# Kernel tuning notes

Hardware: AMD Instinct MI355X
Metric: run time of the kernel (lower is better)

Reference implementation:

```python
import jax, jax.numpy as jnp
import numpy as np

B, N, NODE_DIM = 64, 64, 192
H = 256          # node_hidden_dim
PDIM = 64        # property_embedding_dim
NUM_EDGE_TYPE = 5
T = 4            # message-passing rounds
E = 16384        # total edges (flattened batched graph)
E_SEL = 65536    # selected candidate pairs


def setup_inputs() -> dict:
    key = jax.random.key(0)
    ks = jax.random.split(key, 24)
    def g(k, shape, scale=0.05):
        return jax.random.normal(k, shape, dtype=jnp.float32) * scale
    inp = {
        "x": jax.random.normal(ks[0], (B, N, NODE_DIM), dtype=jnp.float32),
        "edge_index": jax.random.randint(ks[1], (2, E), 0, B * N, dtype=jnp.int32),
        "edge_attr": jax.random.uniform(ks[2], (E, NUM_EDGE_TYPE), dtype=jnp.float32),
        "props": jax.random.normal(ks[3], (B, 1), dtype=jnp.float32),
        "sel_b": jax.random.randint(ks[4], (E_SEL,), 0, B, dtype=jnp.int32),
        "sel_i": jax.random.randint(ks[5], (E_SEL,), 0, N, dtype=jnp.int32),
        "sel_j": jax.random.randint(ks[6], (E_SEL,), 0, N, dtype=jnp.int32),
        "golden_edge": jax.random.randint(ks[7], (E_SEL,), 0, NUM_EDGE_TYPE, dtype=jnp.int32),
        # parameters
        "W_prop": g(ks[8], (1, PDIM)), "b_prop": jnp.zeros((PDIM,), jnp.float32),
        "W_in": g(ks[9], (NODE_DIM, H)), "b_in": jnp.zeros((H,), jnp.float32),
        "W_msg": g(ks[10], (H + NUM_EDGE_TYPE, H)), "b_msg": jnp.zeros((H,), jnp.float32),
        "W_upd": g(ks[11], (2 * H, H)), "b_upd": jnp.zeros((H,), jnp.float32),
        "W_add": g(ks[12], (H + PDIM, H)), "b_add": jnp.zeros((H,), jnp.float32),
        "W1": g(ks[13], (2 * H, H)), "b1": jnp.zeros((H,), jnp.float32),
        "W2": g(ks[14], (H, H)), "b2": jnp.zeros((H,), jnp.float32),
        "W3": g(ks[15], (H, 2 * H)), "b3": jnp.zeros((2 * H,), jnp.float32),
        "W_out": g(ks[16], (2 * H, NUM_EDGE_TYPE)), "b_out": jnp.zeros((NUM_EDGE_TYPE,), jnp.float32),
    }
    return inp


def reference(x, edge_index, edge_attr, props, sel_b, sel_i, sel_j, golden_edge,
              W_prop, b_prop, W_in, b_in, W_msg, b_msg, W_upd, b_upd,
              W_add, b_add, W1, b1, W2, b2, W3, b3, W_out, b_out):
    BN = B * N
    node_x = x.reshape(BN, NODE_DIM)
    src, dst = edge_index[0], edge_index[1]

    # --- GNN node embedding (t rounds of message passing, opaque Encoder.embed_node) ---
    h = jax.nn.relu(node_x @ W_in + b_in)                       # [BN, H]
    for _ in range(T):
        msg_in = jnp.concatenate([h[src], edge_attr], axis=-1)  # [E, H+num_edge_type]
        msg = jax.nn.relu(msg_in @ W_msg + b_msg)               # [E, H]
        agg = jax.ops.segment_sum(msg, dst, num_segments=BN)    # [BN, H]
        h = jax.nn.relu(jnp.concatenate([h, agg], axis=-1) @ W_upd + b_upd)

    node_emb = h.reshape(B, N, H)

    # --- property conditioning + addition linear ---
    prop = props @ W_prop + b_prop                               # [B, PDIM]
    propp = jnp.broadcast_to(prop[:, None, :], (B, N, PDIM))
    node_embg = jnp.concatenate([node_emb, propp], axis=-1) @ W_add + b_add  # [B, N, H]

    # --- gather selected (src, dst) pairs directly (equiv. to repeat_interleave + boolean mask) ---
    flat = node_embg.reshape(BN, H)
    src_e = flat[sel_b * N + sel_i]                              # [E_SEL, H]
    dst_e = flat[sel_b * N + sel_j]                              # [E_SEL, H]
    pair = jnp.concatenate([src_e, dst_e], axis=-1)              # [E_SEL, 2H]

    # --- edge predictor MLP (3 layers, ReLU between) + output linear ---
    h1 = jax.nn.relu(pair @ W1 + b1)
    h2 = jax.nn.relu(h1 @ W2 + b2)
    h3 = h2 @ W3 + b3
    logits = h3 @ W_out + b_out                                  # [E_SEL, num_edge_type]

    # --- cross entropy (mean) ---
    logp = jax.nn.log_softmax(logits, axis=-1)
    loss = -jnp.mean(jnp.take_along_axis(logp, golden_edge[:, None].astype(jnp.int32), axis=-1))
    return loss
```

## Files before the change

### kernel.cpp

```cpp
#include <hip/hip_runtime.h>
#include <math.h>

#define BN 4096
#define N_PER_B 64
#define NE 16384
#define NSEL 65536
#define NET 5
#define PD 64
#define H1STR 260
#define FSTR 264
#define PTILES 4

typedef float f32x4 __attribute__((ext_vector_type(4)));
typedef float f32x16 __attribute__((ext_vector_type(16)));
typedef short short8 __attribute__((ext_vector_type(8)));
typedef short short4v __attribute__((ext_vector_type(4)));

__device__ __forceinline__ unsigned short f2bf(float f) {
    unsigned int u = __builtin_bit_cast(unsigned int, f);
    u += 0x7fff + ((u >> 16) & 1);
    return (unsigned short)(u >> 16);
}
__device__ __forceinline__ float bf_lo(unsigned int u) {
    return __builtin_bit_cast(float, u << 16);
}
__device__ __forceinline__ float bf_hi(unsigned int u) {
    return __builtin_bit_cast(float, u & 0xffff0000u);
}
__device__ __forceinline__ unsigned int pack2(float a, float b) {
    return (unsigned)f2bf(a) | ((unsigned)f2bf(b) << 16);
}
__device__ __forceinline__ short8 ld_frag(const unsigned short* p) {
    const short4v lo = *(const short4v*)(p);
    const short4v hi = *(const short4v*)(p + 4);
    return __builtin_shufflevector(lo, hi, 0, 1, 2, 3, 4, 5, 6, 7);
}
__device__ __forceinline__ unsigned int addrelu2(unsigned int a, unsigned int b, unsigned int c) {
    const float lo = fmaxf(bf_lo(a) + bf_lo(b) + bf_lo(c), 0.f);
    const float hi = fmaxf(bf_hi(a) + bf_hi(b) + bf_hi(c), 0.f);
    return pack2(lo, hi);
}

__global__ __launch_bounds__(256) void k_hist(const int* __restrict__ eidx,
                                              int* __restrict__ deg)
{
    const int e = blockIdx.x * 256 + threadIdx.x;
    atomicAdd(&deg[eidx[NE + e]], 1);
}

__global__ __launch_bounds__(256) void csr_scan(const int* __restrict__ deg,
                                                int* __restrict__ row_start,
                                                int* __restrict__ cursor)
{
    __shared__ int sums[256];
    const int tid = threadIdx.x;
    const int base = tid * 16;
    int local[16];
    int s = 0;
    #pragma unroll
    for (int i = 0; i < 16; ++i) { local[i] = s; s += deg[base + i]; }
    sums[tid] = s;
    __syncthreads();
    for (int off = 1; off < 256; off <<= 1) {
        const int v = sums[tid];
        const int add = (tid >= off) ? sums[tid - off] : 0;
        __syncthreads();
        sums[tid] = v + add;
        __syncthreads();
    }
    const int offset = (tid == 0) ? 0 : sums[tid - 1];
    #pragma unroll
    for (int i = 0; i < 16; ++i) {
        const int v = offset + local[i];
        row_start[base + i] = v;
        cursor[base + i] = v;
    }
    if (tid == 255) row_start[4096] = NE;
}

__global__ __launch_bounds__(256) void csr_scatter(const int* __restrict__ eidx,
                                                   int* __restrict__ cursor,
                                                   int* __restrict__ srcs,
                                                   int* __restrict__ epos)
{
    const int e = blockIdx.x * 256 + threadIdx.x;
    const int pos = atomicAdd(&cursor[eidx[NE + e]], 1);
    srcs[pos] = eidx[e];
    epos[e] = pos;
}

__global__ __launch_bounds__(256) void k_pre(
    const float* __restrict__ W_in, const float* __restrict__ W_msg,
    const float* __restrict__ W_upd, const float* __restrict__ W_add,
    const float* __restrict__ W1, const float* __restrict__ W2,
    const float* __restrict__ W3, const float* __restrict__ b3,
    const float* __restrict__ W_out, const float* __restrict__ b_out,
    const float* __restrict__ props, const float* __restrict__ W_prop,
    const float* __restrict__ b_prop, const float* __restrict__ b_add,
    const float* __restrict__ b_msg, const float* __restrict__ eattr,
    const int* __restrict__ epos,
    unsigned short* __restrict__ wbf, unsigned short* __restrict__ WfT,
    float* __restrict__ bfv, float* __restrict__ prop_add,
    unsigned short* __restrict__ ETc)
{
    __shared__ __align__(16) char smem[16704];
    const int blk = blockIdx.x;
    const int tid = threadIdx.x;

    if (blk < 128) {
        float (*s)[65] = (float(*)[65])smem;
        const int wsel = blk >> 4;
        const int sub = blk & 15;
        const float* src; unsigned short* dst; int K = 256;
        switch (wsel) {
            case 0: src = W_in;              dst = wbf;                         K = 192; break;
            case 1: src = W_msg;             dst = wbf + 49152;                 break;
            case 2: src = W_upd;             dst = wbf + 49152 + 65536;         break;
            case 3: src = W_upd + 256 * 256; dst = wbf + 49152 + 2 * 65536;     break;
            case 4: src = W_add;             dst = wbf + 49152 + 3 * 65536;     break;
            case 5: src = W1;                dst = wbf + 49152 + 4 * 65536;     break;
            case 6: src = W1 + 256 * 256;    dst = wbf + 49152 + 5 * 65536;     break;
            default: src = W2;               dst = wbf + 49152 + 6 * 65536;     break;
        }
        const int k0 = (sub >> 2) * 64;
        const int n0 = (sub & 3) * 64;
        if (k0 >= K) return;
        const int tn = tid & 63;
        const int tg = tid >> 6;
        #pragma unroll
        for (int i = 0; i < 16; ++i) {
            const int kk = tg * 16 + i;
            s[kk][tn] = src[(size_t)(k0 + kk) * 256 + n0 + tn];
        }
        __syncthreads();
        #pragma unroll
        for (int i = 0; i < 16; ++i) {
            const int nn = tg * 16 + i;
            dst[(size_t)(n0 + nn) * K + k0 + tn] = f2bf(s[tn][nn]);
        }
    } else if (blk < 192) {
        const int b = blk - 128;
        const float pv = props[b];
        float acc = b_add[tid];
        for (int p = 0; p < PD; ++p) {
            const float e = fmaf(pv, W_prop[p], b_prop[p]);
            acc = fmaf(e, W_add[(256 + p) * 256 + tid], acc);
        }
        prop_add[b * 256 + tid] = acc;
    } else if (blk < 449) {
        float* part = (float*)smem;
        const int cb = blk - 192;
        float acc[NET] = {0.f, 0.f, 0.f, 0.f, 0.f};
        #pragma unroll
        for (int rep = 0; rep < 2; ++rep) {
            const int j = rep * 256 + tid;
            const float wv = (cb < 256) ? W3[(size_t)cb * 512 + j] : b3[j];
            #pragma unroll
            for (int t = 0; t < NET; ++t) acc[t] = fmaf(wv, W_out[j * NET + t], acc[t]);
        }
        #pragma unroll
        for (int t = 0; t < NET; ++t)
            for (int off = 32; off >= 1; off >>= 1) acc[t] += __shfl_down(acc[t], off);
        if ((tid & 63) == 0) {
            #pragma unroll
            for (int t = 0; t < NET; ++t) part[(tid >> 6) * NET + t] = acc[t];
        }
        __syncthreads();
        if (tid == 0) {
            float s[NET];
            #pragma unroll
            for (int t = 0; t < NET; ++t)
                s[t] = part[t] + part[NET + t] + part[2 * NET + t] + part[3 * NET + t];
            if (cb < 256) {
                #pragma unroll
                for (int t = 0; t < NET; ++t) WfT[t * 256 + cb] = f2bf(s[t]);
                #pragma unroll
                for (int t = NET; t < 16; ++t) WfT[t * 256 + cb] = 0;
            } else {
                #pragma unroll
                for (int t = 0; t < NET; ++t) bfv[t] = s[t] + b_out[t];
            }
        }
    } else {
        float* ea = (float*)smem;
        int* eposs = (int*)(smem + 2560 + 64);
        const int eb = (blk - 449) * 128;
        if (tid < 160)
            *(float4*)&ea[tid * 4] = *(const float4*)(eattr + (size_t)eb * 5 + tid * 4);
        if (tid < 128) eposs[tid] = epos[eb + tid];
        __syncthreads();
        const float* Wme = W_msg + 256 * 256;
        const float w0 = Wme[0 * 256 + tid];
        const float w1 = Wme[1 * 256 + tid];
        const float w2 = Wme[2 * 256 + tid];
        const float w3 = Wme[3 * 256 + tid];
        const float w4 = Wme[4 * 256 + tid];
        const float bm = b_msg[tid];
        for (int i = 0; i < 128; ++i) {
            const float* a = ea + i * 5;
            float v = bm;
            v = fmaf(a[0], w0, v); v = fmaf(a[1], w1, v); v = fmaf(a[2], w2, v);
            v = fmaf(a[3], w3, v); v = fmaf(a[4], w4, v);
            ETc[(size_t)eposs[i] * 256 + tid] = f2bf(v);
        }
    }
}

__global__ __launch_bounds__(1024) void fstep(
    const float* __restrict__ x, const unsigned short* __restrict__ hbuf,
    const unsigned short* __restrict__ Pin, const unsigned short* __restrict__ ETc,
    const int* __restrict__ row_start, const int* __restrict__ srcs,
    const unsigned short* __restrict__ WaT, const unsigned short* __restrict__ WbT,
    const float* __restrict__ bias1,
    const unsigned short* __restrict__ Wp2T, const float* __restrict__ prop_add,
    const unsigned short* __restrict__ W1aT, const unsigned short* __restrict__ W1bT,
    unsigned short* __restrict__ hout, unsigned short* __restrict__ out1,
    unsigned short* __restrict__ out2, int mode)
{
    __shared__ __align__(16) unsigned short Hg[16 * FSTR];
    __shared__ __align__(16) unsigned short Ag[16 * FSTR];
    __shared__ __align__(16) unsigned short Hs[16 * FSTR];
    __shared__ __align__(16) unsigned short H2s[16 * FSTR];
    const int tid = threadIdx.x;
    const int w = tid >> 6;
    const int lane = tid & 63;
    const int q = lane >> 4;
    const int tx = lane & 15;
    const int m0 = blockIdx.x * 16;
    const int col = w * 16 + tx;

    if (mode != 0) {
        {
            const int r = tid >> 6;
            const int c4 = (tid & 63) * 4;
            *(uint2*)&Hg[r * FSTR + c4] =
                *(const uint2*)(hbuf + (size_t)(m0 + r) * 256 + c4);
        }
        {
            const int node = m0 + w;
            const int beg = row_start[node];
            const int end = row_start[node + 1];
            const int c = lane * 4;
            float a0 = 0.f, a1 = 0.f, a2 = 0.f, a3 = 0.f;
            for (int idx = beg; idx < end; ++idx) {
                const int src = srcs[idx];
                const uint2 pu = *(const uint2*)(Pin + (size_t)src * 256 + c);
                const uint2 eu = *(const uint2*)(ETc + (size_t)idx * 256 + c);
                a0 += fmaxf(bf_lo(pu.x) + bf_lo(eu.x), 0.f);
                a1 += fmaxf(bf_hi(pu.x) + bf_hi(eu.x), 0.f);
                a2 += fmaxf(bf_lo(pu.y) + bf_lo(eu.y), 0.f);
                a3 += fmaxf(bf_hi(pu.y) + bf_hi(eu.y), 0.f);
            }
            uint2 o; o.x = pack2(a0, a1); o.y = pack2(a2, a3);
            *(uint2*)&Ag[w * FSTR + c] = o;
        }
        __syncthreads();
    }

    f32x4 acc = (f32x4)0.f;
    if (mode == 0) {
        #pragma unroll
        for (int s = 0; s < 6; ++s) {
            const int k0 = s * 32;
            const float* ap = x + (size_t)(m0 + tx) * 192 + k0 + q * 8;
            const float4 v0 = *(const float4*)ap;
            const float4 v1 = *(const float4*)(ap + 4);
            short8 af;
            af[0] = (short)f2bf(v0.x); af[1] = (short)f2bf(v0.y);
            af[2] = (short)f2bf(v0.z); af[3] = (short)f2bf(v0.w);
            af[4] = (short)f2bf(v1.x); af[5] = (short)f2bf(v1.y);
            af[6] = (short)f2bf(v1.z); af[7] = (short)f2bf(v1.w);
            const short8 bfr = *(const short8*)(WaT + (size_t)col * 192 + k0 + q * 8);
            acc = __builtin_amdgcn_mfma_f32_16x16x32_bf16(af, bfr, acc, 0, 0, 0);
        }
    } else {
        #pragma unroll
        for (int s = 0; s < 8; ++s) {
            const int k0 = s * 32;
            const short8 af = *(const short8*)&Hg[tx * FSTR + k0 + q * 8];
            const short8 bfr = *(const short8*)(WaT + (size_t)col * 256 + k0 + q * 8);
            acc = __builtin_amdgcn_mfma_f32_16x16x32_bf16(af, bfr, acc, 0, 0, 0);
        }
        #pragma unroll
        for (int s = 0; s < 8; ++s) {
            const int k0 = s * 32;
            const short8 af = *(const short8*)&Ag[tx * FSTR + k0 + q * 8];
            const short8 bfr = *(const short8*)(WbT + (size_t)col * 256 + k0 + q * 8);
            acc = __builtin_amdgcn_mfma_f32_16x16x32_bf16(af, bfr, acc, 0, 0, 0);
        }
    }
    {
        const float bv = bias1[col];
        #pragma unroll
        for (int r = 0; r < 4; ++r) {
            const int row = q * 4 + r;
            const unsigned short us = f2bf(fmaxf(acc[r] + bv, 0.f));
            Hs[row * FSTR + col] = us;
            if (mode < 2) hout[(size_t)(m0 + row) * 256 + col] = us;
        }
    }
    __syncthreads();

    acc = (f32x4)0.f;
    #pragma unroll
    for (int s = 0; s < 8; ++s) {
        const int k0 = s * 32;
        const short8 af = *(const short8*)&Hs[tx * FSTR + k0 + q * 8];
        const short8 bfr = *(const short8*)(Wp2T + (size_t)col * 256 + k0 + q * 8);
        acc = __builtin_amdgcn_mfma_f32_16x16x32_bf16(af, bfr, acc, 0, 0, 0);
    }
    if (mode < 2) {
        #pragma unroll
        for (int r = 0; r < 4; ++r)
            out1[(size_t)(m0 + q * 4 + r) * 256 + col] = f2bf(acc[r]);
        return;
    }
    {
        const float pv = prop_add[(m0 >> 6) * 256 + col];
        #pragma unroll
        for (int r = 0; r < 4; ++r)
            H2s[(q * 4 + r) * FSTR + col] = f2bf(acc[r] + pv);
    }
    __syncthreads();

    for (int which = 0; which < 2; ++which) {
        const unsigned short* WT = which ? W1bT : W1aT;
        unsigned short* op = which ? out2 : out1;
        acc = (f32x4)0.f;
        #pragma unroll
        for (int s = 0; s < 8; ++s) {
            const int k0 = s * 32;
            const short8 af = *(const short8*)&H2s[tx * FSTR + k0 + q * 8];
            const short8 bfr = *(const short8*)(WT + (size_t)col * 256 + k0 + q * 8);
            acc = __builtin_amdgcn_mfma_f32_16x16x32_bf16(af, bfr, acc, 0, 0, 0);
        }
        #pragma unroll
        for (int r = 0; r < 4; ++r)
            op[(size_t)(m0 + q * 4 + r) * 256 + col] = f2bf(acc[r]);
    }
}

__global__ __launch_bounds__(512, 1) void pair_k(
    const unsigned short* __restrict__ A1t, const unsigned short* __restrict__ A2t,
    const float* __restrict__ b1, const unsigned short* __restrict__ W2T,
    const float* __restrict__ b2, const unsigned short* __restrict__ WfT,
    const float* __restrict__ bfv,
    const int* __restrict__ sel_b, const int* __restrict__ sel_i,
    const int* __restrict__ sel_j, const int* __restrict__ golden,
    float* __restrict__ out)
{
    __shared__ __align__(16) unsigned short sbuf[64 * H1STR];
    __shared__ __align__(16) unsigned short b1s[256];
    __shared__ float Lg[64 * 8];
    __shared__ int sidx[64 * PTILES], didx[64 * PTILES], gold[64 * PTILES];

    const int tid = threadIdx.x;
    const int w = tid >> 6;
    const int lane = tid & 63;
    const int q = lane >> 4;
    const int tx = lane & 15;
    const int m = lane & 31;
    const int hh = lane >> 5;
    const int e0 = blockIdx.x * 64 * PTILES;

    if (tid < 64 * PTILES) {
        const int e = e0 + tid;
        const int b = sel_b[e];
        sidx[tid] = b * N_PER_B + sel_i[e];
        didx[tid] = b * N_PER_B + sel_j[e];
        gold[tid] = golden[e];
    }
    if (tid < 256) b1s[tid] = f2bf(b1[tid]);

    const int pt = w & 1;
    const int cg = w >> 1;
    short8 Breg[32];
    {
        const unsigned short* bb = W2T + (size_t)(cg * 64 + m) * 256 + hh * 8;
        #pragma unroll
        for (int cc = 0; cc < 2; ++cc)
            #pragma unroll
            for (int s = 0; s < 16; ++s)
                Breg[cc * 16 + s] = *(const short8*)(bb + (size_t)cc * 32 * 256 + s * 16);
    }
    __syncthreads();

    float total = 0.f;

    for (int t = 0; t < PTILES; ++t) {
        {
            const int hw = tid >> 5;
            #pragma unroll
            for (int j = 0; j < 4; ++j) {
                const int p = j * 16 + hw;
                const unsigned short* r1 = A1t + (size_t)sidx[t * 64 + p] * 256 + m * 8;
                const unsigned short* r2 = A2t + (size_t)didx[t * 64 + p] * 256 + m * 8;
                const uint4 u1 = *(const uint4*)r1;
                const uint4 u2 = *(const uint4*)r2;
                const uint4 ub = *(const uint4*)(b1s + m * 8);
                uint2 lo2, hi2;
                lo2.x = addrelu2(u1.x, u2.x, ub.x);
                lo2.y = addrelu2(u1.y, u2.y, ub.y);
                hi2.x = addrelu2(u1.z, u2.z, ub.z);
                hi2.y = addrelu2(u1.w, u2.w, ub.w);
                unsigned short* dbase = sbuf + p * H1STR + m * 8;
                *(uint2*)(dbase) = lo2;
                *(uint2*)(dbase + 4) = hi2;
            }
        }
        __syncthreads();

        f32x16 acc0 = (f32x16)0.f;
        f32x16 acc1 = (f32x16)0.f;
        {
            const unsigned short* arow = sbuf + (size_t)(pt * 32 + m) * H1STR + hh * 8;
            #pragma unroll
            for (int s = 0; s < 16; ++s) {
                const short8 af = ld_frag(arow + s * 16);
                acc0 = __builtin_amdgcn_mfma_f32_32x32x16_bf16(af, Breg[s], acc0, 0, 0, 0);
                acc1 = __builtin_amdgcn_mfma_f32_32x32x16_bf16(af, Breg[16 + s], acc1, 0, 0, 0);
            }
        }
        __syncthreads();

        #pragma unroll
        for (int cc = 0; cc < 2; ++cc) {
            const f32x16* ap = cc ? &acc1 : &acc0;
            const int col = cg * 64 + cc * 32 + m;
            const float bv = b2[col];
            #pragma unroll
            for (int reg = 0; reg < 16; ++reg) {
                const int prow = pt * 32 + (reg & 3) + 8 * (reg >> 2) + 4 * hh;
                sbuf[prow * H1STR + col] = f2bf(fmaxf((*ap)[reg] + bv, 0.f));
            }
        }
        __syncthreads();

        if (w < 4) {
            f32x4 accL = (f32x4)0.f;
            const unsigned short* a2row = sbuf + (size_t)(w * 16 + tx) * H1STR + q * 8;
            const unsigned short* bWf = WfT + (size_t)tx * 256 + q * 8;
            #pragma unroll
            for (int s = 0; s < 8; ++s) {
                const short8 af = ld_frag(a2row + s * 32);
                const short8 bfr = *(const short8*)(bWf + s * 32);
                accL = __builtin_amdgcn_mfma_f32_16x16x32_bf16(af, bfr, accL, 0, 0, 0);
            }
            if (tx < NET) {
                const float bb = bfv[tx];
                #pragma unroll
                for (int reg = 0; reg < 4; ++reg)
                    Lg[(w * 16 + q * 4 + reg) * 8 + tx] = accL[reg] + bb;
            }
        }
        __syncthreads();

        if (tid < 64) {
            float lg[NET];
            #pragma unroll
            for (int tt = 0; tt < NET; ++tt) lg[tt] = Lg[tid * 8 + tt];
            float mx = lg[0];
            #pragma unroll
            for (int tt = 1; tt < NET; ++tt) mx = fmaxf(mx, lg[tt]);
            float s = 0.f;
            #pragma unroll
            for (int tt = 0; tt < NET; ++tt) s += expf(lg[tt] - mx);
            float ls = mx + logf(s) - lg[gold[t * 64 + tid]];
            #pragma unroll
            for (int off = 32; off >= 1; off >>= 1) ls += __shfl_xor(ls, off);
            total += ls;
        }
        __syncthreads();
    }

    if (tid == 0) atomicAdd(out, total * (1.0f / NSEL));
}

extern "C" void kernel_launch(void* const* d_in, const int* in_sizes, int n_in,
                              void* d_out, int out_size, void* d_ws, size_t ws_size,
                              hipStream_t stream) {
    (void)in_sizes; (void)n_in; (void)out_size; (void)ws_size;
    const float* x      = (const float*)d_in[0];
    const int*   eidx   = (const int*)d_in[1];
    const float* eattr  = (const float*)d_in[2];
    const float* props  = (const float*)d_in[3];
    const int*   sel_b  = (const int*)d_in[4];
    const int*   sel_i  = (const int*)d_in[5];
    const int*   sel_j  = (const int*)d_in[6];
    const int*   golden = (const int*)d_in[7];
    const float* W_prop = (const float*)d_in[8];
    const float* b_prop = (const float*)d_in[9];
    const float* W_in   = (const float*)d_in[10];
    const float* b_in   = (const float*)d_in[11];
    const float* W_msg  = (const float*)d_in[12];
    const float* b_msg  = (const float*)d_in[13];
    const float* W_upd  = (const float*)d_in[14];
    const float* b_upd  = (const float*)d_in[15];
    const float* W_add  = (const float*)d_in[16];
    const float* b_add  = (const float*)d_in[17];
    const float* W1     = (const float*)d_in[18];
    const float* b1     = (const float*)d_in[19];
    const float* W2     = (const float*)d_in[20];
    const float* b2     = (const float*)d_in[21];
    const float* W3     = (const float*)d_in[22];
    const float* b3     = (const float*)d_in[23];
    const float* W_out  = (const float*)d_in[24];
    const float* b_out  = (const float*)d_in[25];

    const size_t SEG = (size_t)BN * 256;
    unsigned short* P0   = (unsigned short*)d_ws;
    unsigned short* P1   = P0 + SEG;
    unsigned short* hA   = P1 + SEG;
    unsigned short* hB   = hA + SEG;
    unsigned short* ETc  = hB + SEG;
    unsigned short* wbf  = ETc + (size_t)NE * 256;
    unsigned short* W_inT  = wbf;
    unsigned short* WmT    = wbf + 49152;
    unsigned short* WuaT   = WmT + 65536;
    unsigned short* WubT   = WuaT + 65536;
    unsigned short* W_addT = WubT + 65536;
    unsigned short* W1aT   = W_addT + 65536;
    unsigned short* W1bT   = W1aT + 65536;
    unsigned short* W2T    = W1bT + 65536;
    unsigned short* WfT    = W2T + 65536;
    float* prop_add = (float*)(WfT + 4096);
    float* bfv = prop_add + 64 * 256;
    int* deg       = (int*)(bfv + 16);
    int* row_start = deg + 4096;
    int* cursor    = row_start + 4104;
    int* srcs      = cursor + 4096;
    int* epos      = srcs + NE;

    hipMemsetAsync(deg, 0, 4096 * sizeof(int), stream);
    k_hist<<<NE / 256, 256, 0, stream>>>(eidx, deg);
    csr_scan<<<1, 256, 0, stream>>>(deg, row_start, cursor);
    csr_scatter<<<NE / 256, 256, 0, stream>>>(eidx, cursor, srcs, epos);
    k_pre<<<577, 256, 0, stream>>>(W_in, W_msg, W_upd, W_add, W1, W2, W3, b3,
                                   W_out, b_out, props, W_prop, b_prop, b_add,
                                   b_msg, eattr, epos, wbf, WfT, bfv, prop_add, ETc);

    fstep<<<256, 1024, 0, stream>>>(x, nullptr, nullptr, ETc, row_start, srcs,
                                    W_inT, nullptr, b_in, WmT, nullptr, nullptr, nullptr,
                                    hA, P0, nullptr, 0);
    fstep<<<256, 1024, 0, stream>>>(nullptr, hA, P0, ETc, row_start, srcs,
                                    WuaT, WubT, b_upd, WmT, nullptr, nullptr, nullptr,
                                    hB, P1, nullptr, 1);
    fstep<<<256, 1024, 0, stream>>>(nullptr, hB, P1, ETc, row_start, srcs,
                                    WuaT, WubT, b_upd, WmT, nullptr, nullptr, nullptr,
                                    hA, P0, nullptr, 1);
    fstep<<<256, 1024, 0, stream>>>(nullptr, hA, P0, ETc, row_start, srcs,
                                    WuaT, WubT, b_upd, WmT, nullptr, nullptr, nullptr,
                                    hB, P1, nullptr, 1);
    fstep<<<256, 1024, 0, stream>>>(nullptr, hB, P1, ETc, row_start, srcs,
                                    WuaT, WubT, b_upd, W_addT, prop_add, W1aT, W1bT,
                                    nullptr, P0, hA, 2);

    hipMemsetAsync(d_out, 0, sizeof(float), stream);
    pair_k<<<256, 512, 0, stream>>>(P0, hA, b1, W2T, b2, WfT, bfv,
                                    sel_b, sel_i, sel_j, golden, (float*)d_out);
}
```

Baseline: 252.1 us.

## Fuse message-passing rounds into one persistent kernel with grid barriers

Replaces the five per-round fstep launches with a single persistent kernel of 256 blocks that keeps node hidden states in shared memory and synchronises rounds with an atomic grid barrier. The three CSR-building kernels and the memset are merged into one single-block kernel. Edge-type embeddings are now stored in original edge order and reached through (src, edge) records, so the epos permutation is no longer needed. The memsets of the output and the barrier counter move into k_pre. This removes launch gaps and global round-trips for h, but relies on all 256 blocks being co-resident for the spin barrier, and the CSR build now runs on a single block.

```diff
diff --git a/kernel.cpp b/kernel.cpp
--- a/kernel.cpp
+++ b/kernel.cpp
@@ -41,52 +41,16 @@
     return pack2(lo, hi);
 }
 
-__global__ __launch_bounds__(256) void k_hist(const int* __restrict__ eidx,
-                                              int* __restrict__ deg)
-{
-    const int e = blockIdx.x * 256 + threadIdx.x;
-    atomicAdd(&deg[eidx[NE + e]], 1);
-}
-
-__global__ __launch_bounds__(256) void csr_scan(const int* __restrict__ deg,
-                                                int* __restrict__ row_start,
-                                                int* __restrict__ cursor)
-{
-    __shared__ int sums[256];
-    const int tid = threadIdx.x;
-    const int base = tid * 16;
-    int local[16];
-    int s = 0;
-    #pragma unroll
-    for (int i = 0; i < 16; ++i) { local[i] = s; s += deg[base + i]; }
-    sums[tid] = s;
-    __syncthreads();
-    for (int off = 1; off < 256; off <<= 1) {
-        const int v = sums[tid];
-        const int add = (tid >= off) ? sums[tid - off] : 0;
-        __syncthreads();
-        sums[tid] = v + add;
-        __syncthreads();
-    }
-    const int offset = (tid == 0) ? 0 : sums[tid - 1];
-    #pragma unroll
-    for (int i = 0; i < 16; ++i) {
-        const int v = offset + local[i];
-        row_start[base + i] = v;
-        cursor[base + i] = v;
-    }
-    if (tid == 255) row_start[4096] = NE;
-}
-
-__global__ __launch_bounds__(256) void csr_scatter(const int* __restrict__ eidx,
-                                                   int* __restrict__ cursor,
-                                                   int* __restrict__ srcs,
-                                                   int* __restrict__ epos)
-{
-    const int e = blockIdx.x * 256 + threadIdx.x;
-    const int pos = atomicAdd(&cursor[eidx[NE + e]], 1);
-    srcs[pos] = eidx[e];
-    epos[e] = pos;
+__device__ __forceinline__ void grid_barrier(int* cnt, int target) {
+    __syncthreads();
+    if (threadIdx.x == 0) {
+        __threadfence();
+        __hip_atomic_fetch_add(cnt, 1, __ATOMIC_RELAXED, __HIP_MEMORY_SCOPE_AGENT);
+        while (__hip_atomic_load(cnt, __ATOMIC_RELAXED, __HIP_MEMORY_SCOPE_AGENT) < target)
+            __builtin_amdgcn_s_sleep(2);
+        __threadfence();
+    }
+    __syncthreads();
 }
 
 __global__ __launch_bounds__(256) void k_pre(
@@ -98,10 +62,10 @@
     const float* __restrict__ props, const float* __restrict__ W_prop,
     const float* __restrict__ b_prop, const float* __restrict__ b_add,
     const float* __restrict__ b_msg, const float* __restrict__ eattr,
-    const int* __restrict__ epos,
     unsigned short* __restrict__ wbf, unsigned short* __restrict__ WfT,
     float* __restrict__ bfv, float* __restrict__ prop_add,
-    unsigned short* __restrict__ ETc)
+    unsigned short* __restrict__ ETe, float* __restrict__ dout,
+    int* __restrict__ barcnt)
 {
     __shared__ __align__(16) char smem[16704];
     const int blk = blockIdx.x;
@@ -140,8 +104,10 @@
         }
     } else if (blk < 192) {
         const int b = blk - 128;
+        if (b == 0 && tid == 0) { *dout = 0.f; *barcnt = 0; }
         const float pv = props[b];
         float acc = b_add[tid];
+        #pragma unroll 8
         for (int p = 0; p < PD; ++p) {
             const float e = fmaf(pv, W_prop[p], b_prop[p]);
             acc = fmaf(e, W_add[(256 + p) * 256 + tid], acc);
@@ -183,11 +149,9 @@
         }
     } else {
         float* ea = (float*)smem;
-        int* eposs = (int*)(smem + 2560 + 64);
         const int eb = (blk - 449) * 128;
         if (tid < 160)
             *(float4*)&ea[tid * 4] = *(const float4*)(eattr + (size_t)eb * 5 + tid * 4);
-        if (tid < 128) eposs[tid] = epos[eb + tid];
         __syncthreads();
         const float* Wme = W_msg + 256 * 256;
         const float w0 = Wme[0 * 256 + tid];
@@ -201,25 +165,75 @@
             float v = bm;
             v = fmaf(a[0], w0, v); v = fmaf(a[1], w1, v); v = fmaf(a[2], w2, v);
             v = fmaf(a[3], w3, v); v = fmaf(a[4], w4, v);
-            ETc[(size_t)eposs[i] * 256 + tid] = f2bf(v);
-        }
-    }
-}
-
-__global__ __launch_bounds__(1024) void fstep(
-    const float* __restrict__ x, const unsigned short* __restrict__ hbuf,
-    const unsigned short* __restrict__ Pin, const unsigned short* __restrict__ ETc,
-    const int* __restrict__ row_start, const int* __restrict__ srcs,
-    const unsigned short* __restrict__ WaT, const unsigned short* __restrict__ WbT,
-    const float* __restrict__ bias1,
-    const unsigned short* __restrict__ Wp2T, const float* __restrict__ prop_add,
-    const unsigned short* __restrict__ W1aT, const unsigned short* __restrict__ W1bT,
-    unsigned short* __restrict__ hout, unsigned short* __restrict__ out1,
-    unsigned short* __restrict__ out2, int mode)
+            ETe[(size_t)(eb + i) * 256 + tid] = f2bf(v);
+        }
+    }
+}
+
+__global__ __launch_bounds__(1024) void csr_all(const int* __restrict__ eidx,
+                                                int* __restrict__ row_start,
+                                                int2* __restrict__ recs)
 {
-    __shared__ __align__(16) unsigned short Hg[16 * FSTR];
+    __shared__ int sdeg[4096];
+    __shared__ int scan1[1024];
+    const int tid = threadIdx.x;
+    #pragma unroll
+    for (int i = 0; i < 4; ++i) sdeg[tid * 4 + i] = 0;
+    __syncthreads();
+    #pragma unroll
+    for (int r = 0; r < NE / 1024; ++r)
+        atomicAdd(&sdeg[eidx[NE + r * 1024 + tid]], 1);
+    __syncthreads();
+    const int l0 = sdeg[tid * 4 + 0];
+    const int l1 = sdeg[tid * 4 + 1];
+    const int l2 = sdeg[tid * 4 + 2];
+    const int l3 = sdeg[tid * 4 + 3];
+    scan1[tid] = l0 + l1 + l2 + l3;
+    __syncthreads();
+    for (int off = 1; off < 1024; off <<= 1) {
+        const int v = scan1[tid];
+        const int add = (tid >= off) ? scan1[tid - off] : 0;
+        __syncthreads();
+        scan1[tid] = v + add;
+        __syncthreads();
+    }
+    const int base = (tid == 0) ? 0 : scan1[tid - 1];
+    row_start[tid * 4 + 0] = base;
+    row_start[tid * 4 + 1] = base + l0;
+    row_start[tid * 4 + 2] = base + l0 + l1;
+    row_start[tid * 4 + 3] = base + l0 + l1 + l2;
+    sdeg[tid * 4 + 0] = base;
+    sdeg[tid * 4 + 1] = base + l0;
+    sdeg[tid * 4 + 2] = base + l0 + l1;
+    sdeg[tid * 4 + 3] = base + l0 + l1 + l2;
+    if (tid == 0) row_start[4096] = NE;
+    __syncthreads();
+    #pragma unroll
+    for (int r = 0; r < NE / 1024; ++r) {
+        const int e = r * 1024 + tid;
+        const int d = eidx[NE + e];
+        const int s = eidx[e];
+        const int pos = atomicAdd(&sdeg[d], 1);
+        int2 rec; rec.x = s; rec.y = e;
+        recs[pos] = rec;
+    }
+}
+
+__global__ __launch_bounds__(1024) void mega(
+    const float* __restrict__ x, const unsigned short* __restrict__ ETe,
+    const int* __restrict__ row_start, const int2* __restrict__ recs,
+    const unsigned short* __restrict__ W_inT, const unsigned short* __restrict__ WmT,
+    const unsigned short* __restrict__ WuaT, const unsigned short* __restrict__ WubT,
+    const unsigned short* __restrict__ W_addT, const unsigned short* __restrict__ W1aT,
+    const unsigned short* __restrict__ W1bT,
+    const float* __restrict__ b_in, const float* __restrict__ b_upd,
+    const float* __restrict__ prop_add,
+    unsigned short* __restrict__ P0g, unsigned short* __restrict__ P1g,
+    unsigned short* __restrict__ A2g, int* __restrict__ barcnt)
+{
+    __shared__ __align__(16) unsigned short Ha[16 * FSTR];
+    __shared__ __align__(16) unsigned short Hb[16 * FSTR];
     __shared__ __align__(16) unsigned short Ag[16 * FSTR];
-    __shared__ __align__(16) unsigned short Hs[16 * FSTR];
     __shared__ __align__(16) unsigned short H2s[16 * FSTR];
     const int tid = threadIdx.x;
     const int w = tid >> 6;
@@ -229,36 +243,8 @@
     const int m0 = blockIdx.x * 16;
     const int col = w * 16 + tx;
 
-    if (mode != 0) {
-        {
-            const int r = tid >> 6;
-            const int c4 = (tid & 63) * 4;
-            *(uint2*)&Hg[r * FSTR + c4] =
-                *(const uint2*)(hbuf + (size_t)(m0 + r) * 256 + c4);
-        }
-        {
-            const int node = m0 + w;
-            const int beg = row_start[node];
-            const int end = row_start[node + 1];
-            const int c = lane * 4;
-            float a0 = 0.f, a1 = 0.f, a2 = 0.f, a3 = 0.f;
-            for (int idx = beg; idx < end; ++idx) {
-                const int src = srcs[idx];
-                const uint2 pu = *(const uint2*)(Pin + (size_t)src * 256 + c);
-                const uint2 eu = *(const uint2*)(ETc + (size_t)idx * 256 + c);
-                a0 += fmaxf(bf_lo(pu.x) + bf_lo(eu.x), 0.f);
-                a1 += fmaxf(bf_hi(pu.x) + bf_hi(eu.x), 0.f);
-                a2 += fmaxf(bf_lo(pu.y) + bf_lo(eu.y), 0.f);
-                a3 += fmaxf(bf_hi(pu.y) + bf_hi(eu.y), 0.f);
-            }
-            uint2 o; o.x = pack2(a0, a1); o.y = pack2(a2, a3);
-            *(uint2*)&Ag[w * FSTR + c] = o;
-        }
-        __syncthreads();
-    }
-
-    f32x4 acc = (f32x4)0.f;
-    if (mode == 0) {
+    {
+        f32x4 acc = (f32x4)0.f;
         #pragma unroll
         for (int s = 0; s < 6; ++s) {
             const int k0 = s * 32;
@@ -270,73 +256,135 @@
             af[2] = (short)f2bf(v0.z); af[3] = (short)f2bf(v0.w);
             af[4] = (short)f2bf(v1.x); af[5] = (short)f2bf(v1.y);
             af[6] = (short)f2bf(v1.z); af[7] = (short)f2bf(v1.w);
-            const short8 bfr = *(const short8*)(WaT + (size_t)col * 192 + k0 + q * 8);
+            const short8 bfr = *(const short8*)(W_inT + (size_t)col * 192 + k0 + q * 8);
             acc = __builtin_amdgcn_mfma_f32_16x16x32_bf16(af, bfr, acc, 0, 0, 0);
         }
-    } else {
+        const float bv = b_in[col];
+        #pragma unroll
+        for (int r = 0; r < 4; ++r)
+            Ha[(q * 4 + r) * FSTR + col] = f2bf(fmaxf(acc[r] + bv, 0.f));
+        __syncthreads();
+        acc = (f32x4)0.f;
         #pragma unroll
         for (int s = 0; s < 8; ++s) {
             const int k0 = s * 32;
-            const short8 af = *(const short8*)&Hg[tx * FSTR + k0 + q * 8];
-            const short8 bfr = *(const short8*)(WaT + (size_t)col * 256 + k0 + q * 8);
+            const short8 af = *(const short8*)&Ha[tx * FSTR + k0 + q * 8];
+            const short8 bfr = *(const short8*)(WmT + (size_t)col * 256 + k0 + q * 8);
             acc = __builtin_amdgcn_mfma_f32_16x16x32_bf16(af, bfr, acc, 0, 0, 0);
         }
         #pragma unroll
-        for (int s = 0; s < 8; ++s) {
-            const int k0 = s * 32;
-            const short8 af = *(const short8*)&Ag[tx * FSTR + k0 + q * 8];
-            const short8 bfr = *(const short8*)(WbT + (size_t)col * 256 + k0 + q * 8);
-            acc = __builtin_amdgcn_mfma_f32_16x16x32_bf16(af, bfr, acc, 0, 0, 0);
-        }
-    }
-    {
-        const float bv = bias1[col];
-        #pragma unroll
-        for (int r = 0; r < 4; ++r) {
-            const int row = q * 4 + r;
-            const unsigned short us = f2bf(fmaxf(acc[r] + bv, 0.f));
-            Hs[row * FSTR + col] = us;
-            if (mode < 2) hout[(size_t)(m0 + row) * 256 + col] = us;
-        }
-    }
-    __syncthreads();
-
-    acc = (f32x4)0.f;
-    #pragma unroll
-    for (int s = 0; s < 8; ++s) {
-        const int k0 = s * 32;
-        const short8 af = *(const short8*)&Hs[tx * FSTR + k0 + q * 8];
-        const short8 bfr = *(const short8*)(Wp2T + (size_t)col * 256 + k0 + q * 8);
-        acc = __builtin_amdgcn_mfma_f32_16x16x32_bf16(af, bfr, acc, 0, 0, 0);
-    }
-    if (mode < 2) {
-        #pragma unroll
         for (int r = 0; r < 4; ++r)
-            out1[(size_t)(m0 + q * 4 + r) * 256 + col] = f2bf(acc[r]);
-        return;
-    }
-    {
-        const float pv = prop_add[(m0 >> 6) * 256 + col];
-        #pragma unroll
-        for (int r = 0; r < 4; ++r)
-            H2s[(q * 4 + r) * FSTR + col] = f2bf(acc[r] + pv);
-    }
-    __syncthreads();
-
-    for (int which = 0; which < 2; ++which) {
-        const unsigned short* WT = which ? W1bT : W1aT;
-        unsigned short* op = which ? out2 : out1;
-        acc = (f32x4)0.f;
-        #pragma unroll
-        for (int s = 0; s < 8; ++s) {
-            const int k0 = s * 32;
-            const short8 af = *(const short8*)&H2s[tx * FSTR + k0 + q * 8];
-            const short8 bfr = *(const short8*)(WT + (size_t)col * 256 + k0 + q * 8);
-            acc = __builtin_amdgcn_mfma_f32_16x16x32_bf16(af, bfr, acc, 0, 0, 0);
-        }
-        #pragma unroll
-        for (int r = 0; r < 4; ++r)
-            op[(size_t)(m0 + q * 4 + r) * 256 + col] = f2bf(acc[r]);
+            P0g[(size_t)(m0 + q * 4 + r) * 256 + col] = f2bf(acc[r]);
+    }
+    grid_barrier(barcnt, 256);
+
+    unsigned short* Pr = P0g;
+    unsigned short* Pw = P1g;
+    unsigned short* cur = Ha;
+    unsigned short* nxt = Hb;
+
+    for (int round = 1; round <= 4; ++round) {
+        {
+            const int node = m0 + w;
+            const int beg = row_start[node];
+            const int end = row_start[node + 1];
+            const int c = lane * 4;
+            float a0 = 0.f, a1 = 0.f, a2 = 0.f, a3 = 0.f;
+            int idx = beg;
+            for (; idx + 2 <= end; idx += 2) {
+                const int2 r0 = recs[idx];
+                const int2 r1 = recs[idx + 1];
+                const uint2 p0 = *(const uint2*)(Pr + (size_t)r0.x * 256 + c);
+                const uint2 e0 = *(const uint2*)(ETe + (size_t)r0.y * 256 + c);
+                const uint2 p1 = *(const uint2*)(Pr + (size_t)r1.x * 256 + c);
+                const uint2 e1 = *(const uint2*)(ETe + (size_t)r1.y * 256 + c);
+                a0 += fmaxf(bf_lo(p0.x) + bf_lo(e0.x), 0.f) + fmaxf(bf_lo(p1.x) + bf_lo(e1.x), 0.f);
+                a1 += fmaxf(bf_hi(p0.x) + bf_hi(e0.x), 0.f) + fmaxf(bf_hi(p1.x) + bf_hi(e1.x), 0.f);
+                a2 += fmaxf(bf_lo(p0.y) + bf_lo(e0.y), 0.f) + fmaxf(bf_lo(p1.y) + bf_lo(e1.y), 0.f);
+                a3 += fmaxf(bf_hi(p0.y) + bf_hi(e0.y), 0.f) + fmaxf(bf_hi(p1.y) + bf_hi(e1.y), 0.f);
+            }
+            if (idx < end) {
+                const int2 r0 = recs[idx];
+                const uint2 p0 = *(const uint2*)(Pr + (size_t)r0.x * 256 + c);
+                const uint2 e0 = *(const uint2*)(ETe + (size_t)r0.y * 256 + c);
+                a0 += fmaxf(bf_lo(p0.x) + bf_lo(e0.x), 0.f);
+                a1 += fmaxf(bf_hi(p0.x) + bf_hi(e0.x), 0.f);
+                a2 += fmaxf(bf_lo(p0.y) + bf_lo(e0.y), 0.f);
+                a3 += fmaxf(bf_hi(p0.y) + bf_hi(e0.y), 0.f);
+            }
+            uint2 o; o.x = pack2(a0, a1); o.y = pack2(a2, a3);
+            *(uint2*)&Ag[w * FSTR + c] = o;
+        }
+        __syncthreads();
+
+        {
+            f32x4 acc = (f32x4)0.f;
+            #pragma unroll
+            for (int s = 0; s < 8; ++s) {
+                const int k0 = s * 32;
+                const short8 af = *(const short8*)&cur[tx * FSTR + k0 + q * 8];
+                const short8 bfr = *(const short8*)(WuaT + (size_t)col * 256 + k0 + q * 8);
+                acc = __builtin_amdgcn_mfma_f32_16x16x32_bf16(af, bfr, acc, 0, 0, 0);
+            }
+            #pragma unroll
+            for (int s = 0; s < 8; ++s) {
+                const int k0 = s * 32;
+                const short8 af = *(const short8*)&Ag[tx * FSTR + k0 + q * 8];
+                const short8 bfr = *(const short8*)(WubT + (size_t)col * 256 + k0 + q * 8);
+                acc = __builtin_amdgcn_mfma_f32_16x16x32_bf16(af, bfr, acc, 0, 0, 0);
+            }
+            const float bv = b_upd[col];
+            #pragma unroll
+            for (int r = 0; r < 4; ++r)
+                nxt[(q * 4 + r) * FSTR + col] = f2bf(fmaxf(acc[r] + bv, 0.f));
+        }
+        __syncthreads();
+
+        if (round < 4) {
+            f32x4 acc = (f32x4)0.f;
+            #pragma unroll
+            for (int s = 0; s < 8; ++s) {
+                const int k0 = s * 32;
+                const short8 af = *(const short8*)&nxt[tx * FSTR + k0 + q * 8];
+                const short8 bfr = *(const short8*)(WmT + (size_t)col * 256 + k0 + q * 8);
+                acc = __builtin_amdgcn_mfma_f32_16x16x32_bf16(af, bfr, acc, 0, 0, 0);
+            }
+            #pragma unroll
+            for (int r = 0; r < 4; ++r)
+                Pw[(size_t)(m0 + q * 4 + r) * 256 + col] = f2bf(acc[r]);
+            grid_barrier(barcnt, 256 * (round + 1));
+            unsigned short* t1 = Pr; Pr = Pw; Pw = t1;
+            unsigned short* t2 = cur; cur = nxt; nxt = t2;
+        } else {
+            f32x4 acc = (f32x4)0.f;
+            #pragma unroll
+            for (int s = 0; s < 8; ++s) {
+                const int k0 = s * 32;
+                const short8 af = *(const short8*)&nxt[tx * FSTR + k0 + q * 8];
+                const short8 bfr = *(const short8*)(W_addT + (size_t)col * 256 + k0 + q * 8);
+                acc = __builtin_amdgcn_mfma_f32_16x16x32_bf16(af, bfr, acc, 0, 0, 0);
+            }
+            const float pv = prop_add[(m0 >> 6) * 256 + col];
+            #pragma unroll
+            for (int r = 0; r < 4; ++r)
+                H2s[(q * 4 + r) * FSTR + col] = f2bf(acc[r] + pv);
+            __syncthreads();
+            for (int which = 0; which < 2; ++which) {
+                const unsigned short* WT = which ? W1bT : W1aT;
+                unsigned short* op = which ? A2g : P0g;
+                acc = (f32x4)0.f;
+                #pragma unroll
+                for (int s = 0; s < 8; ++s) {
+                    const int k0 = s * 32;
+                    const short8 af = *(const short8*)&H2s[tx * FSTR + k0 + q * 8];
+                    const short8 bfr = *(const short8*)(WT + (size_t)col * 256 + k0 + q * 8);
+                    acc = __builtin_amdgcn_mfma_f32_16x16x32_bf16(af, bfr, acc, 0, 0, 0);
+                }
+                #pragma unroll
+                for (int r = 0; r < 4; ++r)
+                    op[(size_t)(m0 + q * 4 + r) * 256 + col] = f2bf(acc[r]);
+            }
+        }
     }
 }
 
@@ -510,10 +558,9 @@
     const size_t SEG = (size_t)BN * 256;
     unsigned short* P0   = (unsigned short*)d_ws;
     unsigned short* P1   = P0 + SEG;
-    unsigned short* hA   = P1 + SEG;
-    unsigned short* hB   = hA + SEG;
-    unsigned short* ETc  = hB + SEG;
-    unsigned short* wbf  = ETc + (size_t)NE * 256;
+    unsigned short* A2b  = P1 + SEG;
+    unsigned short* ETe  = A2b + SEG;
+    unsigned short* wbf  = ETe + (size_t)NE * 256;
     unsigned short* W_inT  = wbf;
     unsigned short* WmT    = wbf + 49152;
     unsigned short* WuaT   = WmT + 65536;
@@ -525,37 +572,18 @@
     unsigned short* WfT    = W2T + 65536;
     float* prop_add = (float*)(WfT + 4096);
     float* bfv = prop_add + 64 * 256;
-    int* deg       = (int*)(bfv + 16);
-    int* row_start = deg + 4096;
-    int* cursor    = row_start + 4104;
-    int* srcs      = cursor + 4096;
-    int* epos      = srcs + NE;
-
-    hipMemsetAsync(deg, 0, 4096 * sizeof(int), stream);
-    k_hist<<<NE / 256, 256, 0, stream>>>(eidx, deg);
-    csr_scan<<<1, 256, 0, stream>>>(deg, row_start, cursor);
-    csr_scatter<<<NE / 256, 256, 0, stream>>>(eidx, cursor, srcs, epos);
+    int* barcnt    = (int*)(bfv + 16);
+    int* row_start = barcnt + 16;
+    int2* recs     = (int2*)(row_start + 4104);
+
     k_pre<<<577, 256, 0, stream>>>(W_in, W_msg, W_upd, W_add, W1, W2, W3, b3,
                                    W_out, b_out, props, W_prop, b_prop, b_add,
-                                   b_msg, eattr, epos, wbf, WfT, bfv, prop_add, ETc);
-
-    fstep<<<256, 1024, 0, stream>>>(x, nullptr, nullptr, ETc, row_start, srcs,
-                                    W_inT, nullptr, b_in, WmT, nullptr, nullptr, nullptr,
-                                    hA, P0, nullptr, 0);
-    fstep<<<256, 1024, 0, stream>>>(nullptr, hA, P0, ETc, row_start, srcs,
-                                    WuaT, WubT, b_upd, WmT, nullptr, nullptr, nullptr,
-                                    hB, P1, nullptr, 1);
-    fstep<<<256, 1024, 0, stream>>>(nullptr, hB, P1, ETc, row_start, srcs,
-                                    WuaT, WubT, b_upd, WmT, nullptr, nullptr, nullptr,
-                                    hA, P0, nullptr, 1);
-    fstep<<<256, 1024, 0, stream>>>(nullptr, hA, P0, ETc, row_start, srcs,
-                                    WuaT, WubT, b_upd, WmT, nullptr, nullptr, nullptr,
-                                    hB, P1, nullptr, 1);
-    fstep<<<256, 1024, 0, stream>>>(nullptr, hB, P1, ETc, row_start, srcs,
-                                    WuaT, WubT, b_upd, W_addT, prop_add, W1aT, W1bT,
-                                    nullptr, P0, hA, 2);
-
-    hipMemsetAsync(d_out, 0, sizeof(float), stream);
-    pair_k<<<256, 512, 0, stream>>>(P0, hA, b1, W2T, b2, WfT, bfv,
+                                   b_msg, eattr, wbf, WfT, bfv, prop_add, ETe,
+                                   (float*)d_out, barcnt);
+    csr_all<<<1, 1024, 0, stream>>>(eidx, row_start, recs);
+    mega<<<256, 1024, 0, stream>>>(x, ETe, row_start, recs,
+                                   W_inT, WmT, WuaT, WubT, W_addT, W1aT, W1bT,
+                                   b_in, b_upd, prop_add, P0, P1, A2b, barcnt);
+    pair_k<<<256, 512, 0, stream>>>(P0, A2b, b1, W2T, b2, WfT, bfv,
                                     sel_b, sel_i, sel_j, golden, (float*)d_out);
 }
```

Result: slower. 354.5 us (+40.6%).

## Fuse CSR build into one kernel and balance edge aggregation across block

Applied to the files above, without the earlier changes.

Replaces the memset, histogram, scan and scatter kernels with a single one-block kernel that builds the CSR in shared memory and stores (src,dst) pairs per sorted edge. The output zeroing moves into k_pre, which removes another memset launch. In fstep, each block's 16 waves now stride over all edges of the block's 16 nodes and accumulate into a float shared buffer with atomics, so degree skew no longer leaves most waves idle. The cost is shared-memory atomics, extra shared memory and one more barrier per step, and the CSR build now runs serially on a single block.

```diff
diff --git a/kernel.cpp b/kernel.cpp
--- a/kernel.cpp
+++ b/kernel.cpp
@@ -41,52 +41,55 @@
     return pack2(lo, hi);
 }
 
-__global__ __launch_bounds__(256) void k_hist(const int* __restrict__ eidx,
-                                              int* __restrict__ deg)
+__global__ __launch_bounds__(1024) void csr_all(const int* __restrict__ eidx,
+                                                int* __restrict__ row_start,
+                                                int2* __restrict__ recs,
+                                                int* __restrict__ epos)
 {
-    const int e = blockIdx.x * 256 + threadIdx.x;
-    atomicAdd(&deg[eidx[NE + e]], 1);
-}
-
-__global__ __launch_bounds__(256) void csr_scan(const int* __restrict__ deg,
-                                                int* __restrict__ row_start,
-                                                int* __restrict__ cursor)
-{
-    __shared__ int sums[256];
+    __shared__ int sdeg[4096];
+    __shared__ int scan1[1024];
     const int tid = threadIdx.x;
-    const int base = tid * 16;
-    int local[16];
-    int s = 0;
     #pragma unroll
-    for (int i = 0; i < 16; ++i) { local[i] = s; s += deg[base + i]; }
-    sums[tid] = s;
-    __syncthreads();
-    for (int off = 1; off < 256; off <<= 1) {
-        const int v = sums[tid];
-        const int add = (tid >= off) ? sums[tid - off] : 0;
-        __syncthreads();
-        sums[tid] = v + add;
-        __syncthreads();
-    }
-    const int offset = (tid == 0) ? 0 : sums[tid - 1];
+    for (int i = 0; i < 4; ++i) sdeg[tid * 4 + i] = 0;
+    __syncthreads();
     #pragma unroll
-    for (int i = 0; i < 16; ++i) {
-        const int v = offset + local[i];
-        row_start[base + i] = v;
-        cursor[base + i] = v;
-    }
-    if (tid == 255) row_start[4096] = NE;
-}
-
-__global__ __launch_bounds__(256) void csr_scatter(const int* __restrict__ eidx,
-                                                   int* __restrict__ cursor,
-                                                   int* __restrict__ srcs,
-                                                   int* __restrict__ epos)
-{
-    const int e = blockIdx.x * 256 + threadIdx.x;
-    const int pos = atomicAdd(&cursor[eidx[NE + e]], 1);
-    srcs[pos] = eidx[e];
-    epos[e] = pos;
+    for (int r = 0; r < NE / 1024; ++r)
+        atomicAdd(&sdeg[eidx[NE + r * 1024 + tid]], 1);
+    __syncthreads();
+    const int l0 = sdeg[tid * 4 + 0];
+    const int l1 = sdeg[tid * 4 + 1];
+    const int l2 = sdeg[tid * 4 + 2];
+    const int l3 = sdeg[tid * 4 + 3];
+    scan1[tid] = l0 + l1 + l2 + l3;
+    __syncthreads();
+    for (int off = 1; off < 1024; off <<= 1) {
+        const int v = scan1[tid];
+        const int add = (tid >= off) ? scan1[tid - off] : 0;
+        __syncthreads();
+        scan1[tid] = v + add;
+        __syncthreads();
+    }
+    const int base = (tid == 0) ? 0 : scan1[tid - 1];
+    row_start[tid * 4 + 0] = base;
+    row_start[tid * 4 + 1] = base + l0;
+    row_start[tid * 4 + 2] = base + l0 + l1;
+    row_start[tid * 4 + 3] = base + l0 + l1 + l2;
+    sdeg[tid * 4 + 0] = base;
+    sdeg[tid * 4 + 1] = base + l0;
+    sdeg[tid * 4 + 2] = base + l0 + l1;
+    sdeg[tid * 4 + 3] = base + l0 + l1 + l2;
+    if (tid == 0) row_start[4096] = NE;
+    __syncthreads();
+    #pragma unroll
+    for (int r = 0; r < NE / 1024; ++r) {
+        const int e = r * 1024 + tid;
+        const int d = eidx[NE + e];
+        const int s = eidx[e];
+        const int pos = atomicAdd(&sdeg[d], 1);
+        int2 rec; rec.x = s; rec.y = d;
+        recs[pos] = rec;
+        epos[e] = pos;
+    }
 }
 
 __global__ __launch_bounds__(256) void k_pre(
@@ -101,7 +104,7 @@
     const int* __restrict__ epos,
     unsigned short* __restrict__ wbf, unsigned short* __restrict__ WfT,
     float* __restrict__ bfv, float* __restrict__ prop_add,
-    unsigned short* __restrict__ ETc)
+    unsigned short* __restrict__ ETc, float* __restrict__ dout)
 {
     __shared__ __align__(16) char smem[16704];
     const int blk = blockIdx.x;
@@ -140,8 +143,10 @@
         }
     } else if (blk < 192) {
         const int b = blk - 128;
+        if (b == 0 && tid == 0) *dout = 0.f;
         const float pv = props[b];
         float acc = b_add[tid];
+        #pragma unroll 8
         for (int p = 0; p < PD; ++p) {
             const float e = fmaf(pv, W_prop[p], b_prop[p]);
             acc = fmaf(e, W_add[(256 + p) * 256 + tid], acc);
@@ -209,7 +214,7 @@
 __global__ __launch_bounds__(1024) void fstep(
     const float* __restrict__ x, const unsigned short* __restrict__ hbuf,
     const unsigned short* __restrict__ Pin, const unsigned short* __restrict__ ETc,
-    const int* __restrict__ row_start, const int* __restrict__ srcs,
+    const int* __restrict__ row_start, const int2* __restrict__ recs,
     const unsigned short* __restrict__ WaT, const unsigned short* __restrict__ WbT,
     const float* __restrict__ bias1,
     const unsigned short* __restrict__ Wp2T, const float* __restrict__ prop_add,
@@ -218,6 +223,7 @@
     unsigned short* __restrict__ out2, int mode)
 {
     __shared__ __align__(16) unsigned short Hg[16 * FSTR];
+    __shared__ __align__(16) float Agf[16 * 256];
     __shared__ __align__(16) unsigned short Ag[16 * FSTR];
     __shared__ __align__(16) unsigned short Hs[16 * FSTR];
     __shared__ __align__(16) unsigned short H2s[16 * FSTR];
@@ -230,29 +236,37 @@
     const int col = w * 16 + tx;
 
     if (mode != 0) {
+        #pragma unroll
+        for (int i = 0; i < 4; ++i) Agf[tid * 4 + i] = 0.f;
         {
             const int r = tid >> 6;
             const int c4 = (tid & 63) * 4;
             *(uint2*)&Hg[r * FSTR + c4] =
                 *(const uint2*)(hbuf + (size_t)(m0 + r) * 256 + c4);
         }
+        __syncthreads();
         {
-            const int node = m0 + w;
-            const int beg = row_start[node];
-            const int end = row_start[node + 1];
+            const int beg = row_start[m0];
+            const int end = row_start[m0 + 16];
             const int c = lane * 4;
-            float a0 = 0.f, a1 = 0.f, a2 = 0.f, a3 = 0.f;
-            for (int idx = beg; idx < end; ++idx) {
-                const int src = srcs[idx];
-                const uint2 pu = *(const uint2*)(Pin + (size_t)src * 256 + c);
-                const uint2 eu = *(const uint2*)(ETc + (size_t)idx * 256 + c);
-                a0 += fmaxf(bf_lo(pu.x) + bf_lo(eu.x), 0.f);
-                a1 += fmaxf(bf_hi(pu.x) + bf_hi(eu.x), 0.f);
-                a2 += fmaxf(bf_lo(pu.y) + bf_lo(eu.y), 0.f);
-                a3 += fmaxf(bf_hi(pu.y) + bf_hi(eu.y), 0.f);
-            }
-            uint2 o; o.x = pack2(a0, a1); o.y = pack2(a2, a3);
-            *(uint2*)&Ag[w * FSTR + c] = o;
+            for (int slot = beg + w; slot < end; slot += 16) {
+                const int2 rec = recs[slot];
+                const uint2 pu = *(const uint2*)(Pin + (size_t)rec.x * 256 + c);
+                const uint2 eu = *(const uint2*)(ETc + (size_t)slot * 256 + c);
+                float* arow = Agf + (rec.y - m0) * 256 + c;
+                atomicAdd(arow + 0, fmaxf(bf_lo(pu.x) + bf_lo(eu.x), 0.f));
+                atomicAdd(arow + 1, fmaxf(bf_hi(pu.x) + bf_hi(eu.x), 0.f));
+                atomicAdd(arow + 2, fmaxf(bf_lo(pu.y) + bf_lo(eu.y), 0.f));
+                atomicAdd(arow + 3, fmaxf(bf_hi(pu.y) + bf_hi(eu.y), 0.f));
+            }
+        }
+        __syncthreads();
+        {
+            const int r = tid >> 6;
+            const int c4 = (tid & 63) * 4;
+            const float* s = Agf + r * 256 + c4;
+            uint2 o; o.x = pack2(s[0], s[1]); o.y = pack2(s[2], s[3]);
+            *(uint2*)&Ag[r * FSTR + c4] = o;
         }
         __syncthreads();
     }
@@ -525,37 +539,32 @@
     unsigned short* WfT    = W2T + 65536;
     float* prop_add = (float*)(WfT + 4096);
     float* bfv = prop_add + 64 * 256;
-    int* deg       = (int*)(bfv + 16);
-    int* row_start = deg + 4096;
-    int* cursor    = row_start + 4104;
-    int* srcs      = cursor + 4096;
-    int* epos      = srcs + NE;
-
-    hipMemsetAsync(deg, 0, 4096 * sizeof(int), stream);
-    k_hist<<<NE / 256, 256, 0, stream>>>(eidx, deg);
-    csr_scan<<<1, 256, 0, stream>>>(deg, row_start, cursor);
-    csr_scatter<<<NE / 256, 256, 0, stream>>>(eidx, cursor, srcs, epos);
+    int* row_start = (int*)(bfv + 16);
+    int2* recs     = (int2*)(row_start + 4104);
+    int* epos      = (int*)(recs + NE);
+
+    csr_all<<<1, 1024, 0, stream>>>(eidx, row_start, recs, epos);
     k_pre<<<577, 256, 0, stream>>>(W_in, W_msg, W_upd, W_add, W1, W2, W3, b3,
                                    W_out, b_out, props, W_prop, b_prop, b_add,
-                                   b_msg, eattr, epos, wbf, WfT, bfv, prop_add, ETc);
-
-    fstep<<<256, 1024, 0, stream>>>(x, nullptr, nullptr, ETc, row_start, srcs,
+                                   b_msg, eattr, epos, wbf, WfT, bfv, prop_add,
+                                   ETc, (float*)d_out);
+
+    fstep<<<256, 1024, 0, stream>>>(x, nullptr, nullptr, ETc, row_start, recs,
                                     W_inT, nullptr, b_in, WmT, nullptr, nullptr, nullptr,
                                     hA, P0, nullptr, 0);
-    fstep<<<256, 1024, 0, stream>>>(nullptr, hA, P0, ETc, row_start, srcs,
+    fstep<<<256, 1024, 0, stream>>>(nullptr, hA, P0, ETc, row_start, recs,
                                     WuaT, WubT, b_upd, WmT, nullptr, nullptr, nullptr,
                                     hB, P1, nullptr, 1);
-    fstep<<<256, 1024, 0, stream>>>(nullptr, hB, P1, ETc, row_start, srcs,
+    fstep<<<256, 1024, 0, stream>>>(nullptr, hB, P1, ETc, row_start, recs,
                                     WuaT, WubT, b_upd, WmT, nullptr, nullptr, nullptr,
                                     hA, P0, nullptr, 1);
-    fstep<<<256, 1024, 0, stream>>>(nullptr, hA, P0, ETc, row_start, srcs,
+    fstep<<<256, 1024, 0, stream>>>(nullptr, hA, P0, ETc, row_start, recs,
                                     WuaT, WubT, b_upd, WmT, nullptr, nullptr, nullptr,
                                     hB, P1, nullptr, 1);
-    fstep<<<256, 1024, 0, stream>>>(nullptr, hB, P1, ETc, row_start, srcs,
+    fstep<<<256, 1024, 0, stream>>>(nullptr, hB, P1, ETc, row_start, recs,
                                     WuaT, WubT, b_upd, W_addT, prop_add, W1aT, W1bT,
                                     nullptr, P0, hA, 2);
 
-    hipMemsetAsync(d_out, 0, sizeof(float), stream);
     pair_k<<<256, 512, 0, stream>>>(P0, hA, b1, W2T, b2, WfT, bfv,
                                     sel_b, sel_i, sel_j, golden, (float*)d_out);
 }
```

Result: slower. 354.7 us (+40.7%).
